# Optimization experiments

Measured on AMD Instinct MI355X. Metric: run time of the kernel, lower is better.

## Reference

```python
import jax, jax.numpy as jnp
import numpy as np

B, S, D, FF, H, N, P, K, KP, R = 2, 512, 256, 1024, 4, 512, 32, 16, 4, 64
DH = D // H  # 64


def _ln(x, g, b):
    mu = x.mean(-1, keepdims=True)
    var = ((x - mu) ** 2).mean(-1, keepdims=True)
    return (x - mu) * jax.lax.rsqrt(var + 1e-5) * g + b


def setup_inputs() -> dict:
    key = jax.random.key(0)
    ks = iter(jax.random.split(key, 40))
    nrm = lambda shape, std=0.02: jax.random.normal(next(ks), shape, jnp.float32) * std
    return dict(
        x=jax.random.normal(next(ks), (B, S, D), jnp.float32),
        g1=jnp.ones((D,), jnp.float32), b1=jnp.zeros((D,), jnp.float32),
        g2=jnp.ones((D,), jnp.float32), b2=jnp.zeros((D,), jnp.float32),
        Wq=nrm((D, D)), bq=jnp.zeros((D,), jnp.float32),
        Wk=nrm((D, D)), bk=jnp.zeros((D,), jnp.float32),
        Wv=nrm((D, D)), bv=jnp.zeros((D,), jnp.float32),
        Wpath=nrm((2 * D, 2)), bpath=jnp.zeros((2,), jnp.float32),
        neurons=nrm((N, D)),
        Wnq=nrm((D, D)), bnq=jnp.zeros((D,), jnp.float32),
        Wnk=nrm((D, D)), bnk=jnp.zeros((D,), jnp.float32),
        Wnv=nrm((D, D)), bnv=jnp.zeros((D,), jnp.float32),
        pattern_queries=nrm((P, D)),
        pattern_up_A=nrm((P, D, R)),
        pattern_up_B=nrm((P, R, FF), 0.01),
        Wub=nrm((D, FF), 0.01), bub=jnp.zeros((FF,), jnp.float32),
        Wd=nrm((FF, D), 0.02), bd=jnp.zeros((D,), jnp.float32),
    )


def _forward(x, g1, b1, g2, b2, Wq, bq, Wk, bk, Wv, bv, Wpath, bpath, neurons,
             Wnq, bnq, Wnk, bnk, Wnv, bnv, pattern_queries, pattern_up_A,
             pattern_up_B, Wub, bub, Wd, bd):
    # ---- NeuronRouter on norm1(x) ----
    n1 = _ln(x, g1, b1)
    q = (n1 @ Wq + bq).reshape(B, S, H, DH)
    k = (n1 @ Wk + bk).reshape(B, S, H, DH)
    v = (n1 @ Wv + bv).reshape(B, S, H, DH)
    attn = jax.nn.softmax(jnp.einsum('bqhd,bkhd->bhqk', q, k) / np.float32(np.sqrt(DH)), axis=-1)
    context = jnp.einsum('bhqk,bkhd->bqhd', attn, v).reshape(B, S, D)
    token_scores = n1 @ neurons.T        # [B,S,N]
    context_scores = context @ neurons.T
    w = jax.nn.softmax(jnp.concatenate([n1, context], -1) @ Wpath + bpath, axis=-1)
    scores = w[..., 0:1] * token_scores + w[..., 1:2] * context_scores
    topk_scores, topk_idx = jax.lax.top_k(scores, K)
    topk_w = jax.nn.softmax(topk_scores, axis=-1)      # [B,S,K]
    selected = neurons[topk_idx]                        # [B,S,K,D]

    # ---- InteractionFFN on norm2(x) ----
    n2 = _ln(x, g2, b2)
    qn = (selected @ Wnq + bnq).reshape(B, S, K, H, DH)
    kn = (selected @ Wnk + bnk).reshape(B, S, K, H, DH)
    vn = jax.nn.sigmoid((selected @ Wnv + bnv).reshape(B, S, K, H, DH))
    aw = jax.nn.softmax(jnp.einsum('bsqhd,bskhd->bshqk', qn, kn) / np.float32(np.sqrt(DH)), axis=-1)
    gates = jnp.einsum('bshqk,bskhd->bsqhd', aw, vn).reshape(B, S, K, D)
    aggregated = jnp.sum(topk_w[..., None] * (selected * gates), axis=2)  # [B,S,D]

    pattern_scores = 0.5 * (aggregated @ pattern_queries.T) / np.float32(np.sqrt(D)) \
                     + 0.5 * (context @ pattern_queries.T)               # [B,S,P]
    tps, tpi = jax.lax.top_k(pattern_scores, KP)
    tpw = jax.nn.softmax(tps, axis=-1)                                   # [B,S,KP]

    combined = n2 + aggregated
    A = pattern_up_A[tpi]    # [B,S,KP,D,R]  (gathered per-token LoRA A)
    Bm = pattern_up_B[tpi]   # [B,S,KP,R,FF] (gathered per-token LoRA B)
    h_mid = jnp.einsum('bsd,bskdr->bskr', combined, A)
    h_pat = jnp.einsum('bskr,bskrf->bskf', h_mid, Bm)
    h_pattern = jnp.sum(tpw[..., None] * h_pat, axis=2)                  # [B,S,FF]
    h = jax.nn.gelu(0.1 * (combined @ Wub + bub) + 0.9 * h_pattern, approximate=False)
    out = h @ Wd + bd
    return x + out, topk_idx


def reference(x, g1, b1, g2, b2, Wq, bq, Wk, bk, Wv, bv, Wpath, bpath, neurons,
              Wnq, bnq, Wnk, bnk, Wnv, bnv, pattern_queries, pattern_up_A,
              pattern_up_B, Wub, bub, Wd, bd):
    return _forward(x, g1, b1, g2, b2, Wq, bq, Wk, bk, Wv, bv, Wpath, bpath,
                    neurons, Wnq, bnq, Wnk, bnk, Wnv, bnv, pattern_queries,
                    pattern_up_A, pattern_up_B, Wub, bub, Wd, bd)
```

## Files before the change

kernel.cpp:

```cpp
#include <hip/hip_runtime.h>
#include <hip/hip_bf16.h>
#include <math.h>

#define BB 2
#define SS 512
#define DD 256
#define FFD 1024
#define HH 4
#define NN 512
#define PP 32
#define KK 16
#define KPP 4
#define RR 64
#define DHH 64
#define TT (BB*SS)
#define QT 16

__global__ __launch_bounds__(256) void ln_kernel(
    const float* __restrict__ x,
    const float* __restrict__ g1, const float* __restrict__ b1,
    const float* __restrict__ g2, const float* __restrict__ b2,
    float* __restrict__ n1, float* __restrict__ n2,
    int* __restrict__ binc)
{
    int t = blockIdx.x;
    int d = threadIdx.x;
    if (t == 0 && d < 32) binc[d] = 0;
    __shared__ float red[256];
    float v = x[t*DD + d];
    red[d] = v; __syncthreads();
    for (int s = 128; s > 0; s >>= 1) { if (d < s) red[d] += red[d+s]; __syncthreads(); }
    float mu = red[0] * (1.0f/DD);
    __syncthreads();
    float dv = v - mu;
    red[d] = dv*dv; __syncthreads();
    for (int s = 128; s > 0; s >>= 1) { if (d < s) red[d] += red[d+s]; __syncthreads(); }
    float var = red[0] * (1.0f/DD);
    float r = 1.0f / sqrtf(var + 1e-5f);
    n1[t*DD+d] = dv*r*g1[d] + b1[d];
    n2[t*DD+d] = dv*r*g2[d] + b2[d];
}

__device__ __forceinline__ void gemm_body(
    const float* __restrict__ A, const float* __restrict__ Bm,
    const float* __restrict__ bias, const float* __restrict__ extra,
    float* __restrict__ C, int M, int Nn, int Kk, int transB, int mode,
    int k0off, int kLen)
{
    __shared__ float As[2][32][68];
    __shared__ float Bs[2][32][68];
    int bm = blockIdx.y * 64;
    int bn = blockIdx.x * 64;
    int tid = threadIdx.x;
    int tx = tid & 15, ty = tid >> 4;

    float4 pa[2], pb[2];

    #define LOAD_A(kbase) { \
        _Pragma("unroll") \
        for (int e = 0; e < 2; ++e) { \
            int r = e*32 + (tid>>3); int c4 = tid & 7; \
            pa[e] = *(const float4*)&A[(size_t)(bm + r)*Kk + (kbase) + c4*4]; \
        } }
    #define STORE_A(buf) { \
        _Pragma("unroll") \
        for (int e = 0; e < 2; ++e) { \
            int r = e*32 + (tid>>3); int c4 = tid & 7; \
            As[buf][c4*4+0][r] = pa[e].x; \
            As[buf][c4*4+1][r] = pa[e].y; \
            As[buf][c4*4+2][r] = pa[e].z; \
            As[buf][c4*4+3][r] = pa[e].w; \
        } }
    #define LOAD_B(kbase) { \
        if (transB == 0) { \
            _Pragma("unroll") \
            for (int e = 0; e < 2; ++e) { \
                int c = e*16 + (tid>>4); int n4 = tid & 15; \
                pb[e] = *(const float4*)&Bm[(size_t)((kbase) + c)*Nn + bn + n4*4]; \
            } \
        } else { \
            _Pragma("unroll") \
            for (int e = 0; e < 2; ++e) { \
                int r = e*32 + (tid>>3); int k4 = tid & 7; \
                pb[e] = *(const float4*)&Bm[(size_t)(bn + r)*Kk + (kbase) + k4*4]; \
            } \
        } }
    #define STORE_B(buf) { \
        if (transB == 0) { \
            _Pragma("unroll") \
            for (int e = 0; e < 2; ++e) { \
                int c = e*16 + (tid>>4); int n4 = tid & 15; \
                *(float4*)&Bs[buf][c][n4*4] = pb[e]; \
            } \
        } else { \
            _Pragma("unroll") \
            for (int e = 0; e < 2; ++e) { \
                int r = e*32 + (tid>>3); int k4 = tid & 7; \
                Bs[buf][k4*4+0][r] = pb[e].x; \
                Bs[buf][k4*4+1][r] = pb[e].y; \
                Bs[buf][k4*4+2][r] = pb[e].z; \
                Bs[buf][k4*4+3][r] = pb[e].w; \
            } \
        } }

    float acc[4][4] = {};
    int nk = kLen >> 5;

    LOAD_A(k0off); LOAD_B(k0off);
    STORE_A(0); STORE_B(0);
    __syncthreads();

    for (int kt = 0; kt < nk; ++kt) {
        int cur = kt & 1;
        if (kt + 1 < nk) { LOAD_A(k0off + (kt+1)*32); LOAD_B(k0off + (kt+1)*32); }
        #pragma unroll
        for (int kk = 0; kk < 32; ++kk) {
            float4 av = *(const float4*)&As[cur][kk][ty*4];
            float4 bv = *(const float4*)&Bs[cur][kk][tx*4];
            acc[0][0] = fmaf(av.x, bv.x, acc[0][0]);
            acc[0][1] = fmaf(av.x, bv.y, acc[0][1]);
            acc[0][2] = fmaf(av.x, bv.z, acc[0][2]);
            acc[0][3] = fmaf(av.x, bv.w, acc[0][3]);
            acc[1][0] = fmaf(av.y, bv.x, acc[1][0]);
            acc[1][1] = fmaf(av.y, bv.y, acc[1][1]);
            acc[1][2] = fmaf(av.y, bv.z, acc[1][2]);
            acc[1][3] = fmaf(av.y, bv.w, acc[1][3]);
            acc[2][0] = fmaf(av.z, bv.x, acc[2][0]);
            acc[2][1] = fmaf(av.z, bv.y, acc[2][1]);
            acc[2][2] = fmaf(av.z, bv.z, acc[2][2]);
            acc[2][3] = fmaf(av.z, bv.w, acc[2][3]);
            acc[3][0] = fmaf(av.w, bv.x, acc[3][0]);
            acc[3][1] = fmaf(av.w, bv.y, acc[3][1]);
            acc[3][2] = fmaf(av.w, bv.z, acc[3][2]);
            acc[3][3] = fmaf(av.w, bv.w, acc[3][3]);
        }
        if (kt + 1 < nk) {
            STORE_A(cur^1); STORE_B(cur^1);
            __syncthreads();
        }
    }

    #pragma unroll
    for (int i = 0; i < 4; ++i) {
        int m = bm + ty*4 + i;
        #pragma unroll
        for (int j = 0; j < 4; ++j) {
            int n = bn + tx*4 + j;
            float val = acc[i][j] + (bias ? bias[n] : 0.0f);
            if (mode == 1) {
                val = 1.0f / (1.0f + expf(-val));
            } else if (mode == 2) {
                size_t idx = (size_t)m*Nn + n;
                float hp = extra[idx] + extra[idx + (size_t)TT*FFD]
                         + extra[idx + 2*(size_t)TT*FFD] + extra[idx + 3*(size_t)TT*FFD];
                float z = 0.1f*val + 0.9f*hp;
                val = 0.5f*z*(1.0f + erff(z*0.70710678118654752f));
            } else if (mode == 3) {
                val = val + extra[(size_t)m*Nn+n];
            }
            C[(size_t)m*Nn + n] = val;
        }
    }
    #undef LOAD_A
    #undef STORE_A
    #undef LOAD_B
    #undef STORE_B
}

__global__ __launch_bounds__(256) void gemm_kernel(
    const float* __restrict__ A, const float* __restrict__ Bm,
    const float* __restrict__ bias, const float* __restrict__ extra,
    float* __restrict__ C, int M, int Nn, int Kk, int transB, int mode)
{
    gemm_body(A, Bm, bias, extra, C, M, Nn, Kk, transB, mode, 0, Kk);
}

struct GemmSet { const float* A; const float* B; const float* bias; float* C; int mode; int M; };

__global__ __launch_bounds__(256) void gemm2_kernel(
    GemmSet s0, GemmSet s1, int Nn, int Kk, int transB)
{
    GemmSet s = (blockIdx.z == 0) ? s0 : s1;
    if ((int)blockIdx.y * 64 >= s.M) return;
    gemm_body(s.A, s.B, s.bias, nullptr, s.C, s.M, Nn, Kk, transB, s.mode, 0, Kk);
}

__global__ __launch_bounds__(256) void gemm6_kernel(
    GemmSet s0, GemmSet s1, GemmSet s2, GemmSet s3, GemmSet s4, GemmSet s5,
    int Nn, int Kk, int transB)
{
    GemmSet s;
    switch (blockIdx.z) {
        case 0: s = s0; break;
        case 1: s = s1; break;
        case 2: s = s2; break;
        case 3: s = s3; break;
        case 4: s = s4; break;
        default: s = s5; break;
    }
    if ((int)blockIdx.y * 64 >= s.M) return;
    gemm_body(s.A, s.B, s.bias, nullptr, s.C, s.M, Nn, Kk, transB, s.mode, 0, Kk);
}

__global__ __launch_bounds__(256) void gemm_splitk_kernel(
    const float* __restrict__ A, const float* __restrict__ Bm,
    float* __restrict__ Cpart, int M, int Nn, int Kk, int kPerSplit)
{
    int sk = blockIdx.z;
    float* Cp = Cpart + (size_t)sk * M * Nn;
    gemm_body(A, Bm, nullptr, nullptr, Cp, M, Nn, Kk, 0, 0, sk*kPerSplit, kPerSplit);
}

__global__ __launch_bounds__(256) void combine_wd_kernel(
    const float* __restrict__ part, const float* __restrict__ x,
    const float* __restrict__ bd, float* __restrict__ out)
{
    int i = blockIdx.x*256 + threadIdx.x;
    int d = i & (DD-1);
    float s = x[i] + bd[d];
    s += part[i] + part[i + TT*DD] + part[i + 2*TT*DD] + part[i + 3*TT*DD];
    out[i] = s;
}

__global__ __launch_bounds__(256) void attn_kernel(
    const float* __restrict__ q, const float* __restrict__ k,
    const float* __restrict__ v, float* __restrict__ ctx)
{
    int bi = blockIdx.x;
    int qt = bi & 31;
    int bh = bi >> 5;
    int h = bh & (HH-1);
    int b = bh >> 2;
    int tid = threadIdx.x;
    int qo = tid >> 4;
    int c  = tid & 15;

    __shared__ float Qs[QT][68];
    __shared__ float Kt[64][64];
    __shared__ float Vs[64][68];
    __shared__ float Ps[QT][68];

    {
        const float* qp = q + ((size_t)(b*SS + qt*QT + qo)*DD) + h*DHH + c*4;
        *(float4*)&Qs[qo][c*4] = *(const float4*)qp;
    }
    float O0=0.f, O1=0.f, O2=0.f, O3=0.f;
    float mreg = -3.4e38f, lreg = 0.f;

    for (int t = 0; t < 8; ++t) {
        if (t) __syncthreads();
        #pragma unroll
        for (int e = 0; e < 4; ++e) {
            int lin = e*256 + tid;
            int kr = lin & 63;
            int c4 = lin >> 6;
            const float* kp = k + ((size_t)(b*SS + t*64 + kr)*DD) + h*DHH + c4*4;
            float4 kv = *(const float4*)kp;
            Kt[c4*4+0][kr] = kv.x;
            Kt[c4*4+1][kr] = kv.y;
            Kt[c4*4+2][kr] = kv.z;
            Kt[c4*4+3][kr] = kv.w;
            int vr = lin >> 4;
            int vc = lin & 15;
            const float* vp = v + ((size_t)(b*SS + t*64 + vr)*DD) + h*DHH + vc*4;
            *(float4*)&Vs[vr][vc*4] = *(const float4*)vp;
        }
        __syncthreads();
        float s0=0.f, s1=0.f, s2=0.f, s3=0.f;
        #pragma unroll 8
        for (int d = 0; d < 64; ++d) {
            float qv = Qs[qo][d];
            float4 kv = *(const float4*)&Kt[d][c*4];
            s0 = fmaf(qv, kv.x, s0);
            s1 = fmaf(qv, kv.y, s1);
            s2 = fmaf(qv, kv.z, s2);
            s3 = fmaf(qv, kv.w, s3);
        }
        s0 *= 0.125f; s1 *= 0.125f; s2 *= 0.125f; s3 *= 0.125f;
        float mx = fmaxf(fmaxf(s0, s1), fmaxf(s2, s3));
        #pragma unroll
        for (int mk = 1; mk <= 8; mk <<= 1)
            mx = fmaxf(mx, __shfl_xor(mx, mk));
        float mnew = fmaxf(mreg, mx);
        float scl = __expf(mreg - mnew);
        float e0 = __expf(s0 - mnew), e1 = __expf(s1 - mnew),
              e2 = __expf(s2 - mnew), e3 = __expf(s3 - mnew);
        float esum = e0 + e1 + e2 + e3;
        #pragma unroll
        for (int mk = 1; mk <= 8; mk <<= 1)
            esum += __shfl_xor(esum, mk);
        lreg = lreg * scl + esum;
        mreg = mnew;
        float4 pw; pw.x = e0; pw.y = e1; pw.z = e2; pw.w = e3;
        *(float4*)&Ps[qo][c*4] = pw;
        __syncthreads();
        O0 *= scl; O1 *= scl; O2 *= scl; O3 *= scl;
        #pragma unroll 8
        for (int kk = 0; kk < 64; ++kk) {
            float pv = Ps[qo][kk];
            float4 vv = *(const float4*)&Vs[kk][c*4];
            O0 = fmaf(pv, vv.x, O0);
            O1 = fmaf(pv, vv.y, O1);
            O2 = fmaf(pv, vv.z, O2);
            O3 = fmaf(pv, vv.w, O3);
        }
    }
    float linv = 1.0f / lreg;
    float4 o4; o4.x = O0*linv; o4.y = O1*linv; o4.z = O2*linv; o4.w = O3*linv;
    *(float4*)(ctx + ((size_t)(b*SS + qt*QT + qo)*DD) + h*DHH + c*4) = o4;
}

__global__ __launch_bounds__(256) void token_kernel(
    const float* __restrict__ n1, const float* __restrict__ ctx,
    const float* __restrict__ Wpath, const float* __restrict__ bpath,
    const float* __restrict__ ts, const float* __restrict__ cs,
    const float* __restrict__ neurons,
    const float* __restrict__ nqa, const float* __restrict__ nka,
    const float* __restrict__ nva,
    const float* __restrict__ n2p, const float* __restrict__ PQ,
    float* __restrict__ comb_out, float* __restrict__ tpwg,
    int* __restrict__ tpib,
    int* __restrict__ binc, int* __restrict__ bine,
    float* __restrict__ out_idx)
{
    int t = blockIdx.x, tid = threadIdx.x;
    int wv = tid >> 6;

    __shared__ float sc[NN];
    __shared__ float pw0[4], pw1[4];
    __shared__ float w0s, w1s;
    __shared__ float wvv[4]; __shared__ int wvi[4];
    __shared__ float selv[KK]; __shared__ int seli[KK];
    __shared__ float tw[KK];
    __shared__ float nq[KK][DD+1];
    __shared__ float nk[KK][DD+1];
    __shared__ float nv[KK][DD+1];
    __shared__ float ps[HH][KK][KK];
    __shared__ float mix[DD];
    __shared__ float psp[8][33];
    __shared__ float pts[PP];
    __shared__ int tpi[KPP];

    float a = n1[t*DD+tid], c = ctx[t*DD+tid];

    {
        float r0 = a * Wpath[tid*2+0] + c * Wpath[(DD+tid)*2+0];
        float r1 = a * Wpath[tid*2+1] + c * Wpath[(DD+tid)*2+1];
        #pragma unroll
        for (int off = 1; off < 64; off <<= 1) {
            r0 += __shfl_xor(r0, off);
            r1 += __shfl_xor(r1, off);
        }
        if ((tid & 63) == 0) { pw0[wv] = r0; pw1[wv] = r1; }
    }
    __syncthreads();
    if (tid == 0) {
        float l0 = pw0[0]+pw0[1]+pw0[2]+pw0[3] + bpath[0];
        float l1 = pw1[0]+pw1[1]+pw1[2]+pw1[3] + bpath[1];
        float mm = fmaxf(l0, l1);
        float e0 = expf(l0-mm), e1 = expf(l1-mm);
        float is = 1.0f/(e0+e1);
        w0s = e0*is; w1s = e1*is;
    }
    __syncthreads();
    {
        float w0 = w0s, w1 = w1s;
        sc[tid]     = w0*ts[t*NN+tid]     + w1*cs[t*NN+tid];
        sc[tid+256] = w0*ts[t*NN+tid+256] + w1*cs[t*NN+tid+256];
    }
    __syncthreads();
    for (int it = 0; it < KK; ++it) {
        float v0 = sc[tid], v1 = sc[tid+256];
        float bv; int bi;
        if (v0 >= v1) { bv = v0; bi = tid; } else { bv = v1; bi = tid+256; }
        #pragma unroll
        for (int off = 1; off < 64; off <<= 1) {
            float ov = __shfl_xor(bv, off);
            int   oi = __shfl_xor(bi, off);
            if (ov > bv || (ov == bv && oi < bi)) { bv = ov; bi = oi; }
        }
        if ((tid & 63) == 0) { wvv[wv] = bv; wvi[wv] = bi; }
        __syncthreads();
        if (tid == 0) {
            float fv = wvv[0]; int fi = wvi[0];
            #pragma unroll
            for (int w = 1; w < 4; ++w) {
                float ov = wvv[w]; int oi = wvi[w];
                if (ov > fv || (ov == fv && oi < fi)) { fv = ov; fi = oi; }
            }
            selv[it] = fv; seli[it] = fi; sc[fi] = -3.4e38f;
        }
        __syncthreads();
    }
    if (tid == 0) {
        float mx = selv[0];
        float e[KK]; float sum = 0.f;
        for (int i = 0; i < KK; ++i) { e[i] = expf(selv[i]-mx); sum += e[i]; }
        float is = 1.0f/sum;
        for (int i = 0; i < KK; ++i) {
            tw[i] = e[i]*is;
            out_idx[t*KK+i] = (float)seli[i];
        }
    }
    __syncthreads();

    for (int i = 0; i < KK; ++i) {
        int idx = seli[i];
        nq[i][tid] = nqa[idx*DD+tid];
        nk[i][tid] = nka[idx*DD+tid];
        nv[i][tid] = nva[idx*DD+tid];
    }
    __syncthreads();
    #pragma unroll
    for (int r = 0; r < 4; ++r) {
        int lin = r*256 + tid;
        int j = lin & 15, i = (lin >> 4) & 15, h = lin >> 8;
        const float* qp = &nq[i][h*DHH];
        const float* kp = &nk[j][h*DHH];
        float acc = 0.f;
        #pragma unroll 8
        for (int d = 0; d < DHH; ++d) acc = fmaf(qp[d], kp[d], acc);
        ps[h][i][j] = acc * 0.125f;
    }
    __syncthreads();
    if (tid < 64) {
        int h = tid >> 4, i = tid & 15;
        float mx = -3.4e38f;
        for (int j = 0; j < KK; ++j) mx = fmaxf(mx, ps[h][i][j]);
        float sum = 0.f;
        for (int j = 0; j < KK; ++j) { float e = expf(ps[h][i][j]-mx); ps[h][i][j] = e; sum += e; }
        float is = 1.0f/sum;
        for (int j = 0; j < KK; ++j) ps[h][i][j] *= is;
    }
    __syncthreads();
    float agg = 0.f;
    {
        int d = tid, h = d >> 6;
        for (int i = 0; i < KK; ++i) {
            float g = 0.f;
            #pragma unroll
            for (int j = 0; j < KK; ++j) g = fmaf(ps[h][i][j], nv[j][d], g);
            agg += tw[i] * neurons[seli[i]*DD + d] * g;
        }
    }

    mix[tid] = 0.03125f * agg + 0.5f * c;
    float cb = n2p[t*DD+tid] + agg;
    comb_out[t*DD+tid] = cb;
    __syncthreads();
    {
        int p = tid & 31, g = tid >> 5;
        const float* pq = PQ + p*DD + g*32;
        const float* mp = mix + g*32;
        float acc = 0.f;
        #pragma unroll
        for (int d = 0; d < 32; ++d) acc = fmaf(mp[d], pq[d], acc);
        psp[g][p] = acc;
    }
    __syncthreads();
    if (tid < PP) {
        float s = 0.f;
        #pragma unroll
        for (int g = 0; g < 8; ++g) s += psp[g][tid];
        pts[tid] = s;
    }
    __syncthreads();
    if (tid == 0) {
        float vals[KPP];
        #pragma unroll
        for (int it = 0; it < KPP; ++it) {
            float bv = -3.4e38f; int bi = 0;
            for (int p = 0; p < PP; ++p) { float v = pts[p]; if (v > bv) { bv = v; bi = p; } }
            vals[it] = bv; tpi[it] = bi; pts[bi] = -3.4e38f;
        }
        float mx = vals[0];
        float e0 = expf(vals[0]-mx), e1 = expf(vals[1]-mx),
              e2 = expf(vals[2]-mx), e3 = expf(vals[3]-mx);
        float is = 1.0f/(e0+e1+e2+e3);
        tpwg[t*4+0]=e0*is; tpwg[t*4+1]=e1*is; tpwg[t*4+2]=e2*is; tpwg[t*4+3]=e3*is;
    }
    __syncthreads();
    if (tid < KPP) {
        int p = tpi[tid];
        tpib[t*4+tid] = p;
        int slot = atomicAdd(&binc[p], 1);
        bine[p*TT + slot] = (t << 2) | tid;
    }
}

__global__ __launch_bounds__(256) void hmid_kernel(
    const float* __restrict__ comb, const float* __restrict__ tpwg,
    const int* __restrict__ tpib, const float* __restrict__ Aup,
    float* __restrict__ hmid_g)
{
    int t = blockIdx.x, tid = threadIdx.x;
    __shared__ float combs[DD];
    combs[tid] = comb[(size_t)t*DD + tid];
    __syncthreads();
    int kp = tid >> 6, r = tid & 63;
    int p = tpib[t*4 + kp];
    const float* Ap = Aup + (size_t)p*(DD*RR) + r;
    float acc = 0.f;
    #pragma unroll 8
    for (int d = 0; d < DD; ++d)
        acc = fmaf(combs[d], Ap[(size_t)d*RR], acc);
    hmid_g[(size_t)(t*4 + kp)*RR + r] = acc * tpwg[t*4 + kp];
}

__global__ __launch_bounds__(256) void lora_apply(
    const int* __restrict__ bin_count, const int* __restrict__ bin_entry,
    const float* __restrict__ hmid_g, const float* __restrict__ Bup,
    float* __restrict__ hpat4)
{
    int p = blockIdx.x, ff0 = blockIdx.y * 128;
    int base = blockIdx.z * 64;
    int cnt = bin_count[p];
    if (base >= cnt) return;
    int nt = cnt - base; if (nt > 64) nt = 64;
    int tid = threadIdx.x;

    __shared__ float Bs[RR][132];
    __shared__ float hmT[RR][68];
    __shared__ int es[64];

    const float* Bp = Bup + (size_t)p*(RR*FFD) + ff0;
    #pragma unroll
    for (int e = 0; e < 8; ++e) {
        int lin = e*256 + tid;
        int r = lin >> 5, cg = lin & 31;
        *(float4*)&Bs[r][cg*4] = *(const float4*)&Bp[(size_t)r*FFD + cg*4];
    }
    if (tid < 64) es[tid] = (tid < nt) ? bin_entry[p*TT + base + tid] : -1;
    __syncthreads();
    #pragma unroll
    for (int e = 0; e < 4; ++e) {
        int lin = e*256 + tid;
        int i = lin >> 4, rg = lin & 15;
        int ei = es[i];
        float4 hv = make_float4(0.f,0.f,0.f,0.f);
        if (ei >= 0) hv = *(const float4*)&hmid_g[(size_t)ei*RR + rg*4];
        hmT[rg*4+0][i] = hv.x;
        hmT[rg*4+1][i] = hv.y;
        hmT[rg*4+2][i] = hv.z;
        hmT[rg*4+3][i] = hv.w;
    }
    __syncthreads();

    int eg = tid >> 5, cg = tid & 31;
    float4 acc[8];
    #pragma unroll
    for (int j = 0; j < 8; ++j) acc[j] = make_float4(0.f,0.f,0.f,0.f);
    #pragma unroll 4
    for (int r = 0; r < RR; ++r) {
        float4 b  = *(const float4*)&Bs[r][cg*4];
        float4 h0 = *(const float4*)&hmT[r][eg*8];
        float4 h1 = *(const float4*)&hmT[r][eg*8+4];
        acc[0].x = fmaf(h0.x, b.x, acc[0].x); acc[0].y = fmaf(h0.x, b.y, acc[0].y);
        acc[0].z = fmaf(h0.x, b.z, acc[0].z); acc[0].w = fmaf(h0.x, b.w, acc[0].w);
        acc[1].x = fmaf(h0.y, b.x, acc[1].x); acc[1].y = fmaf(h0.y, b.y, acc[1].y);
        acc[1].z = fmaf(h0.y, b.z, acc[1].z); acc[1].w = fmaf(h0.y, b.w, acc[1].w);
        acc[2].x = fmaf(h0.z, b.x, acc[2].x); acc[2].y = fmaf(h0.z, b.y, acc[2].y);
        acc[2].z = fmaf(h0.z, b.z, acc[2].z); acc[2].w = fmaf(h0.z, b.w, acc[2].w);
        acc[3].x = fmaf(h0.w, b.x, acc[3].x); acc[3].y = fmaf(h0.w, b.y, acc[3].y);
        acc[3].z = fmaf(h0.w, b.z, acc[3].z); acc[3].w = fmaf(h0.w, b.w, acc[3].w);
        acc[4].x = fmaf(h1.x, b.x, acc[4].x); acc[4].y = fmaf(h1.x, b.y, acc[4].y);
        acc[4].z = fmaf(h1.x, b.z, acc[4].z); acc[4].w = fmaf(h1.x, b.w, acc[4].w);
        acc[5].x = fmaf(h1.y, b.x, acc[5].x); acc[5].y = fmaf(h1.y, b.y, acc[5].y);
        acc[5].z = fmaf(h1.y, b.z, acc[5].z); acc[5].w = fmaf(h1.y, b.w, acc[5].w);
        acc[6].x = fmaf(h1.z, b.x, acc[6].x); acc[6].y = fmaf(h1.z, b.y, acc[6].y);
        acc[6].z = fmaf(h1.z, b.z, acc[6].z); acc[6].w = fmaf(h1.z, b.w, acc[6].w);
        acc[7].x = fmaf(h1.w, b.x, acc[7].x); acc[7].y = fmaf(h1.w, b.y, acc[7].y);
        acc[7].z = fmaf(h1.w, b.z, acc[7].z); acc[7].w = fmaf(h1.w, b.w, acc[7].w);
    }
    #pragma unroll
    for (int j = 0; j < 8; ++j) {
        int e = es[eg*8+j];
        if (e >= 0) {
            int t = e >> 2, kp = e & 3;
            *(float4*)&hpat4[(size_t)kp*(TT*FFD) + (size_t)t*FFD + ff0 + cg*4] = acc[j];
        }
    }
}

extern "C" void kernel_launch(void* const* d_in, const int* in_sizes, int n_in,
                              void* d_out, int out_size, void* d_ws, size_t ws_size,
                              hipStream_t stream)
{
    const float* x        = (const float*)d_in[0];
    const float* g1       = (const float*)d_in[1];
    const float* b1       = (const float*)d_in[2];
    const float* g2       = (const float*)d_in[3];
    const float* b2       = (const float*)d_in[4];
    const float* Wq       = (const float*)d_in[5];
    const float* bq       = (const float*)d_in[6];
    const float* Wk       = (const float*)d_in[7];
    const float* bk       = (const float*)d_in[8];
    const float* Wv       = (const float*)d_in[9];
    const float* bv       = (const float*)d_in[10];
    const float* Wpath    = (const float*)d_in[11];
    const float* bpath    = (const float*)d_in[12];
    const float* neurons  = (const float*)d_in[13];
    const float* Wnq      = (const float*)d_in[14];
    const float* bnq      = (const float*)d_in[15];
    const float* Wnk      = (const float*)d_in[16];
    const float* bnk      = (const float*)d_in[17];
    const float* Wnv      = (const float*)d_in[18];
    const float* bnv      = (const float*)d_in[19];
    const float* PQ       = (const float*)d_in[20];
    const float* Aup      = (const float*)d_in[21];
    const float* Bup      = (const float*)d_in[22];
    const float* Wub      = (const float*)d_in[23];
    const float* bub      = (const float*)d_in[24];
    const float* Wd       = (const float*)d_in[25];
    const float* bd       = (const float*)d_in[26];

    float* out0    = (float*)d_out;
    float* out_idx = out0 + (size_t)TT*DD;

    float* ws = (float*)d_ws;
    float* n1    = ws; ws += TT*DD;
    float* n2    = ws; ws += TT*DD;
    float* qb    = ws; ws += TT*DD;
    float* kb    = ws; ws += TT*DD;
    float* vb    = ws; ws += TT*DD;
    float* ctx   = ws; ws += TT*DD;
    float* ts    = ws; ws += TT*NN;
    float* cs    = ws; ws += TT*NN;
    float* nqa   = ws; ws += NN*DD;
    float* nka   = ws; ws += NN*DD;
    float* nva   = ws; ws += NN*DD;
    float* comb  = ws; ws += TT*DD;
    float* hpat4 = ws; ws += 4*TT*FFD;
    float* hb    = ws; ws += TT*FFD;
    float* part  = ws; ws += 4*TT*DD;
    float* hmidg = ws; ws += 4*TT*RR;
    float* tpwg  = ws; ws += TT*KPP;
    int*   tpib  = (int*)ws; ws += TT*KPP;
    int*   binc  = (int*)ws; ws += 32;
    int*   bine  = (int*)ws; ws += 32*TT;

    dim3 blk(256);

    ln_kernel<<<TT, blk, 0, stream>>>(x, g1, b1, g2, b2, n1, n2, binc);

    {
        GemmSet sq{n1, Wq, bq, qb, 0, TT}, sk{n1, Wk, bk, kb, 0, TT},
                sv{n1, Wv, bv, vb, 0, TT},
                p0{neurons, Wnq, bnq, nqa, 0, NN}, p1{neurons, Wnk, bnk, nka, 0, NN},
                p2{neurons, Wnv, bnv, nva, 1, NN};
        gemm6_kernel<<<dim3(DD/64, TT/64, 6), blk, 0, stream>>>(sq, sk, sv, p0, p1, p2, DD, DD, 0);
    }

    attn_kernel<<<BB*HH*(SS/QT), blk, 0, stream>>>(qb, kb, vb, ctx);

    {
        GemmSet s0{n1, neurons, nullptr, ts, 0, TT}, s1{ctx, neurons, nullptr, cs, 0, TT};
        gemm2_kernel<<<dim3(NN/64, TT/64, 2), blk, 0, stream>>>(s0, s1, NN, DD, 1);
    }

    token_kernel<<<TT, blk, 0, stream>>>(n1, ctx, Wpath, bpath, ts, cs,
                                         neurons, nqa, nka, nva, n2, PQ,
                                         comb, tpwg, tpib, binc, bine, out_idx);

    hmid_kernel<<<TT, blk, 0, stream>>>(comb, tpwg, tpib, Aup, hmidg);

    lora_apply<<<dim3(PP, FFD/128, 16), blk, 0, stream>>>(binc, bine, hmidg, Bup, hpat4);

    gemm_kernel<<<dim3(FFD/64, TT/64), blk, 0, stream>>>(comb, Wub, bub, hpat4, hb, TT, FFD, DD, 0, 2);

    gemm_splitk_kernel<<<dim3(DD/64, TT/64, 4), blk, 0, stream>>>(hb, Wd, part, TT, DD, FFD, FFD/4);
    combine_wd_kernel<<<TT*DD/256, blk, 0, stream>>>(part, x, bd, out0);
}
```

Measured before the change: 346.7 us.

## Do router top-k in a single wavefront with register shuffles

The 16-way neuron top-k is moved from a block-wide loop, which needed two barriers per iteration and a shared score array, into one 64-lane wavefront. Each lane keeps 8 scores in registers and reduces them with xor shuffles. The pattern top-4 now uses 32-lane shuffles instead of a serial scan by thread 0. The nq shared tile is removed and Q is read straight from global memory to cut LDS use, at the cost of redundant global reads and other waves idling during selection.

```diff
diff --git a/kernel.cpp b/kernel.cpp
--- a/kernel.cpp
+++ b/kernel.cpp
@@ -326,20 +326,15 @@
     int t = blockIdx.x, tid = threadIdx.x;
     int wv = tid >> 6;
 
-    __shared__ float sc[NN];
-    __shared__ float pw0[4], pw1[4];
-    __shared__ float w0s, w1s;
-    __shared__ float wvv[4]; __shared__ int wvi[4];
-    __shared__ float selv[KK]; __shared__ int seli[KK];
-    __shared__ float tw[KK];
-    __shared__ float nq[KK][DD+1];
     __shared__ float nk[KK][DD+1];
     __shared__ float nv[KK][DD+1];
     __shared__ float ps[HH][KK][KK];
     __shared__ float mix[DD];
     __shared__ float psp[8][33];
-    __shared__ float pts[PP];
-    __shared__ int tpi[KPP];
+    __shared__ float pw0[4], pw1[4];
+    __shared__ float w01[2];
+    __shared__ float selv[KK]; __shared__ int seli[KK];
+    __shared__ float tw[KK];
 
     float a = n1[t*DD+tid], c = ctx[t*DD+tid];
 
@@ -360,67 +355,82 @@
         float mm = fmaxf(l0, l1);
         float e0 = expf(l0-mm), e1 = expf(l1-mm);
         float is = 1.0f/(e0+e1);
-        w0s = e0*is; w1s = e1*is;
-    }
-    __syncthreads();
-    {
-        float w0 = w0s, w1 = w1s;
-        sc[tid]     = w0*ts[t*NN+tid]     + w1*cs[t*NN+tid];
-        sc[tid+256] = w0*ts[t*NN+tid+256] + w1*cs[t*NN+tid+256];
-    }
-    __syncthreads();
-    for (int it = 0; it < KK; ++it) {
-        float v0 = sc[tid], v1 = sc[tid+256];
-        float bv; int bi;
-        if (v0 >= v1) { bv = v0; bi = tid; } else { bv = v1; bi = tid+256; }
-        #pragma unroll
-        for (int off = 1; off < 64; off <<= 1) {
-            float ov = __shfl_xor(bv, off);
-            int   oi = __shfl_xor(bi, off);
-            if (ov > bv || (ov == bv && oi < bi)) { bv = ov; bi = oi; }
-        }
-        if ((tid & 63) == 0) { wvv[wv] = bv; wvi[wv] = bi; }
-        __syncthreads();
+        w01[0] = e0*is; w01[1] = e1*is;
+    }
+    __syncthreads();
+
+    if (tid < 64) {
+        float w0 = w01[0], w1 = w01[1];
+        const float* tsp = ts + (size_t)t*NN;
+        const float* csp = cs + (size_t)t*NN;
+        float s0 = w0*tsp[tid      ] + w1*csp[tid      ];
+        float s1 = w0*tsp[tid +  64] + w1*csp[tid +  64];
+        float s2 = w0*tsp[tid + 128] + w1*csp[tid + 128];
+        float s3 = w0*tsp[tid + 192] + w1*csp[tid + 192];
+        float s4 = w0*tsp[tid + 256] + w1*csp[tid + 256];
+        float s5 = w0*tsp[tid + 320] + w1*csp[tid + 320];
+        float s6 = w0*tsp[tid + 384] + w1*csp[tid + 384];
+        float s7 = w0*tsp[tid + 448] + w1*csp[tid + 448];
+        #pragma unroll
+        for (int it = 0; it < KK; ++it) {
+            float bv = s0; int bc = 0;
+            if (s1 > bv) { bv = s1; bc = 1; }
+            if (s2 > bv) { bv = s2; bc = 2; }
+            if (s3 > bv) { bv = s3; bc = 3; }
+            if (s4 > bv) { bv = s4; bc = 4; }
+            if (s5 > bv) { bv = s5; bc = 5; }
+            if (s6 > bv) { bv = s6; bc = 6; }
+            if (s7 > bv) { bv = s7; bc = 7; }
+            int bi = bc*64 + tid;
+            #pragma unroll
+            for (int off = 1; off < 64; off <<= 1) {
+                float ov = __shfl_xor(bv, off);
+                int   oi = __shfl_xor(bi, off);
+                if (ov > bv || (ov == bv && oi < bi)) { bv = ov; bi = oi; }
+            }
+            if ((bi & 63) == tid) {
+                switch (bi >> 6) {
+                    case 0: s0 = -3.4e38f; break;
+                    case 1: s1 = -3.4e38f; break;
+                    case 2: s2 = -3.4e38f; break;
+                    case 3: s3 = -3.4e38f; break;
+                    case 4: s4 = -3.4e38f; break;
+                    case 5: s5 = -3.4e38f; break;
+                    case 6: s6 = -3.4e38f; break;
+                    default: s7 = -3.4e38f; break;
+                }
+            }
+            if (tid == 0) { selv[it] = bv; seli[it] = bi; }
+        }
         if (tid == 0) {
-            float fv = wvv[0]; int fi = wvi[0];
+            float mx = selv[0];
+            float e[KK]; float sum = 0.f;
             #pragma unroll
-            for (int w = 1; w < 4; ++w) {
-                float ov = wvv[w]; int oi = wvi[w];
-                if (ov > fv || (ov == fv && oi < fi)) { fv = ov; fi = oi; }
-            }
-            selv[it] = fv; seli[it] = fi; sc[fi] = -3.4e38f;
-        }
-        __syncthreads();
-    }
-    if (tid == 0) {
-        float mx = selv[0];
-        float e[KK]; float sum = 0.f;
-        for (int i = 0; i < KK; ++i) { e[i] = expf(selv[i]-mx); sum += e[i]; }
-        float is = 1.0f/sum;
-        for (int i = 0; i < KK; ++i) {
-            tw[i] = e[i]*is;
-            out_idx[t*KK+i] = (float)seli[i];
-        }
-    }
-    __syncthreads();
+            for (int i = 0; i < KK; ++i) { e[i] = expf(selv[i]-mx); sum += e[i]; }
+            float is = 1.0f/sum;
+            #pragma unroll
+            for (int i = 0; i < KK; ++i) tw[i] = e[i]*is;
+        }
+    }
+    __syncthreads();
+
+    if (tid < KK) out_idx[t*KK + tid] = (float)seli[tid];
 
     for (int i = 0; i < KK; ++i) {
         int idx = seli[i];
-        nq[i][tid] = nqa[idx*DD+tid];
         nk[i][tid] = nka[idx*DD+tid];
         nv[i][tid] = nva[idx*DD+tid];
     }
     __syncthreads();
     #pragma unroll
     for (int r = 0; r < 4; ++r) {
-        int lin = r*256 + tid;
-        int j = lin & 15, i = (lin >> 4) & 15, h = lin >> 8;
-        const float* qp = &nq[i][h*DHH];
-        const float* kp = &nk[j][h*DHH];
+        int j = tid & 15, i = tid >> 4;
+        const float* qg = nqa + (size_t)seli[i]*DD + r*DHH;
+        const float* kp = &nk[j][r*DHH];
         float acc = 0.f;
         #pragma unroll 8
-        for (int d = 0; d < DHH; ++d) acc = fmaf(qp[d], kp[d], acc);
-        ps[h][i][j] = acc * 0.125f;
+        for (int d = 0; d < DHH; ++d) acc = fmaf(qg[d], kp[d], acc);
+        ps[r][i][j] = acc * 0.125f;
     }
     __syncthreads();
     if (tid < 64) {
@@ -458,33 +468,33 @@
         psp[g][p] = acc;
     }
     __syncthreads();
-    if (tid < PP) {
-        float s = 0.f;
-        #pragma unroll
-        for (int g = 0; g < 8; ++g) s += psp[g][tid];
-        pts[tid] = s;
-    }
-    __syncthreads();
-    if (tid == 0) {
-        float vals[KPP];
-        #pragma unroll
-        for (int it = 0; it < KPP; ++it) {
-            float bv = -3.4e38f; int bi = 0;
-            for (int p = 0; p < PP; ++p) { float v = pts[p]; if (v > bv) { bv = v; bi = p; } }
-            vals[it] = bv; tpi[it] = bi; pts[bi] = -3.4e38f;
-        }
-        float mx = vals[0];
-        float e0 = expf(vals[0]-mx), e1 = expf(vals[1]-mx),
-              e2 = expf(vals[2]-mx), e3 = expf(vals[3]-mx);
-        float is = 1.0f/(e0+e1+e2+e3);
-        tpwg[t*4+0]=e0*is; tpwg[t*4+1]=e1*is; tpwg[t*4+2]=e2*is; tpwg[t*4+3]=e3*is;
-    }
-    __syncthreads();
-    if (tid < KPP) {
-        int p = tpi[tid];
-        tpib[t*4+tid] = p;
-        int slot = atomicAdd(&binc[p], 1);
-        bine[p*TT + slot] = (t << 2) | tid;
+    if (tid < 32) {
+        float sv = 0.f;
+        #pragma unroll
+        for (int g = 0; g < 8; ++g) sv += psp[g][tid];
+        float v0, v1, v2, v3; int i0, i1, i2, i3;
+        #define TOP1(VV, II) { \
+            float bv = sv; int bi = tid; \
+            _Pragma("unroll") \
+            for (int off = 1; off < 32; off <<= 1) { \
+                float ov = __shfl_xor(bv, off); \
+                int   oi = __shfl_xor(bi, off); \
+                if (ov > bv || (ov == bv && oi < bi)) { bv = ov; bi = oi; } \
+            } \
+            if (bi == tid) sv = -3.4e38f; \
+            VV = bv; II = bi; }
+        TOP1(v0, i0) TOP1(v1, i1) TOP1(v2, i2) TOP1(v3, i3)
+        #undef TOP1
+        if (tid < KPP) {
+            float vs = (tid==0) ? v0 : (tid==1) ? v1 : (tid==2) ? v2 : v3;
+            int   pi = (tid==0) ? i0 : (tid==1) ? i1 : (tid==2) ? i2 : i3;
+            float e0 = expf(v0-v0), e1 = expf(v1-v0), e2 = expf(v2-v0), e3 = expf(v3-v0);
+            float is = 1.0f/(e0+e1+e2+e3);
+            tpwg[t*4+tid] = expf(vs - v0) * is;
+            tpib[t*4+tid] = pi;
+            int slot = atomicAdd(&binc[pi], 1);
+            bine[pi*TT + slot] = (t << 2) | tid;
+        }
     }
 }
 
```

After: 331.6 us. 1.05x faster.
